# Kernel tuning notes

Hardware: AMD Instinct MI355X
Metric: run time of the kernel (lower is better)

Reference implementation:

```python
import jax, jax.numpy as jnp
import numpy as np

C = 384; NH = 12; HD = C // NH; MLP = int(C * 4.0)
B = 8; T = 12; N = 256; BT = B * T
EPS = 1e-6


def _ln(x):
    # LayerNorm without affine, eps=1e-6
    mu = jnp.mean(x, axis=-1, keepdims=True)
    var = jnp.mean(jnp.square(x - mu), axis=-1, keepdims=True)
    return (x - mu) / jnp.sqrt(var + EPS)


def _attention(x, wqkv, bqkv, wproj, bproj, bias=None):
    b, n, c = x.shape
    qkv = (x @ wqkv.T + bqkv).reshape(b, n, 3, NH, HD)
    q = qkv[:, :, 0].transpose(0, 2, 1, 3)  # [b,h,n,d]
    k = qkv[:, :, 1].transpose(0, 2, 1, 3)
    v = qkv[:, :, 2].transpose(0, 2, 1, 3)
    attn = jnp.einsum('bhnd,bhmd->bhnm', q, k) * (HD ** -0.5)
    if bias is not None:
        attn = attn + bias
    attn = jax.nn.softmax(attn, axis=-1)
    out = jnp.einsum('bhnm,bhmd->bhnd', attn, v).transpose(0, 2, 1, 3).reshape(b, n, c)
    return out @ wproj.T + bproj, attn


def setup_inputs() -> dict:
    key = jax.random.key(0)
    ks = jax.random.split(key, 20)
    s = 0.02
    inp = {
        'x': jax.random.normal(ks[0], (BT, N, C), jnp.float32),
        'c': jax.random.normal(ks[1], (BT, C), jnp.float32),
        'rel_pos_bias': jax.random.normal(ks[2], (1, NH, N, N), jnp.float32) * s,
        'w_adaln': jax.random.normal(ks[3], (9 * C, C), jnp.float32) * s,
        'b_adaln': jnp.zeros((9 * C,), jnp.float32),
        'wqkv_s': jax.random.normal(ks[4], (3 * C, C), jnp.float32) * s,
        'bqkv_s': jnp.zeros((3 * C,), jnp.float32),
        'wproj_s': jax.random.normal(ks[5], (C, C), jnp.float32) * s,
        'bproj_s': jnp.zeros((C,), jnp.float32),
        'wqkv_t': jax.random.normal(ks[6], (3 * C, C), jnp.float32) * s,
        'bqkv_t': jnp.zeros((3 * C,), jnp.float32),
        'wproj_t': jax.random.normal(ks[7], (C, C), jnp.float32) * s,
        'bproj_t': jnp.zeros((C,), jnp.float32),
        'w1': jax.random.normal(ks[8], (MLP, C), jnp.float32) * s,
        'b1': jnp.zeros((MLP,), jnp.float32),
        'w2': jax.random.normal(ks[9], (C, MLP), jnp.float32) * s,
        'b2': jnp.zeros((C,), jnp.float32),
        'T_pred': T,
    }
    return inp


def reference(x, c, rel_pos_bias, w_adaln, b_adaln, wqkv_s, bqkv_s, wproj_s, bproj_s,
              wqkv_t, bqkv_t, wproj_t, bproj_t, w1, b1, w2, b2, T_pred):
    mod = jax.nn.silu(c) @ w_adaln.T + b_adaln  # [BT, 9C]
    (shift_s, scale_s, gate_s, shift_t, scale_t, gate_t,
     shift_mlp, scale_mlp, gate_mlp) = jnp.split(mod, 9, axis=1)

    # spatial attention with adaLN modulate + gate
    x_mod = _ln(x) * (1 + scale_s[:, None]) + shift_s[:, None]
    x_s, attn_map = _attention(x_mod, wqkv_s, bqkv_s, wproj_s, bproj_s, bias=rel_pos_bias)
    x = x + gate_s[:, None] * x_s

    if T_pred > 1:
        bt, n, cdim = x.shape
        b = bt // T_pred
        xt = x.reshape(b, T_pred, n, cdim).transpose(0, 2, 1, 3).reshape(b * n, T_pred, cdim)
        sc = scale_t.reshape(b, 1, T_pred, cdim)
        sh = shift_t.reshape(b, 1, T_pred, cdim)
        gt = gate_t.reshape(b, 1, T_pred, cdim)
        norm_t = _ln(xt).reshape(b, n, T_pred, cdim)
        mod_t = (norm_t * (1 + sc) + sh).reshape(b * n, T_pred, cdim)
        x_t, _ = _attention(mod_t, wqkv_t, bqkv_t, wproj_t, bproj_t)
        x_t = (x_t.reshape(b, n, T_pred, cdim) * gt).transpose(0, 2, 1, 3).reshape(bt, n, cdim)
        x = x + x_t

    # gated MLP with exact (erf) GELU, matching nn.GELU default
    h = _ln(x) * (1 + scale_mlp[:, None]) + shift_mlp[:, None]
    h = jax.nn.gelu(h @ w1.T + b1, approximate=False) @ w2.T + b2
    x = x + gate_mlp[:, None] * h
    return (x, attn_map)
```

## Files before the change

### kernel.cpp

```cpp
#include <hip/hip_runtime.h>
#include <hip/hip_bf16.h>
#include <math.h>

typedef __bf16 bf16;
typedef __bf16 bf16x8 __attribute__((ext_vector_type(8)));
typedef __bf16 bf16x4 __attribute__((ext_vector_type(4)));
typedef float  f32x4  __attribute__((ext_vector_type(4)));

#define C_    384
#define NH_   12
#define HD_   32
#define MLP_  1536
#define B_    8
#define T_    12
#define N_    256
#define BT_   96
#define M_    24576
#define NINE_C 3456
#define QKV_  1152

#define GLOAD16(gptr, lptr)                                                \
  __builtin_amdgcn_global_load_lds(                                       \
      (const __attribute__((address_space(1))) void*)(gptr),              \
      (__attribute__((address_space(3))) void*)(lptr), 16, 0, 0)

__device__ __forceinline__ float wave_sum(float v) {
#pragma unroll
  for (int o = 32; o > 0; o >>= 1) v += __shfl_xor(v, o, 64);
  return v;
}

template <typename TO> __device__ __forceinline__ TO to_out(float v);
template <> __device__ __forceinline__ float to_out<float>(float v) { return v; }
template <> __device__ __forceinline__ bf16  to_out<bf16>(float v)  { return (bf16)v; }

struct F2BArgs {
  const float* src[7];
  bf16* dst[7];
  int n4[7];
};
__global__ __launch_bounds__(256) void k_f2b_all(F2BArgs a) {
  const int seg = blockIdx.y;
  const int i = blockIdx.x * 256 + threadIdx.x;
  if (i < a.n4[seg]) {
    float4 v = ((const float4*)a.src[seg])[i];
    bf16x4 o;
    o[0] = (bf16)v.x; o[1] = (bf16)v.y; o[2] = (bf16)v.z; o[3] = (bf16)v.w;
    ((bf16x4*)a.dst[seg])[i] = o;
  }
}

__global__ __launch_bounds__(384) void k_silu(const float* __restrict__ c,
                                              bf16* __restrict__ out) {
  const int row = blockIdx.x, tid = threadIdx.x;
  float v = 0.f;
  if (row < BT_) {
    float cv = c[row * C_ + tid];
    v = cv / (1.f + __expf(-cv));
  }
  out[row * C_ + tid] = (bf16)v;
}

__global__ __launch_bounds__(256) void k_ln_mod(const float* __restrict__ x,
                                                const float* __restrict__ mod,
                                                bf16* __restrict__ out,
                                                int shift_chunk, int scale_chunk) {
  const int wave = threadIdx.x >> 6, lane = threadIdx.x & 63;
  const int r = blockIdx.x * 4 + wave;
  const float* xr = x + (size_t)r * C_;
  float v[6];
  float s = 0.f, ss = 0.f;
#pragma unroll
  for (int e = 0; e < 6; ++e) { v[e] = xr[lane + 64 * e]; s += v[e]; ss += v[e] * v[e]; }
  s = wave_sum(s); ss = wave_sum(ss);
  const float mean = s * (1.f / C_);
  const float var  = ss * (1.f / C_) - mean * mean;
  const float rs   = rsqrtf(var + 1e-6f);
  const int bt = r >> 8;
  const float* sh = mod + (size_t)bt * NINE_C + shift_chunk * C_;
  const float* sc = mod + (size_t)bt * NINE_C + scale_chunk * C_;
  bf16* orow = out + (size_t)r * C_;
#pragma unroll
  for (int e = 0; e < 6; ++e) {
    int cc = lane + 64 * e;
    orow[cc] = (bf16)((v[e] - mean) * rs * (1.f + sc[cc]) + sh[cc]);
  }
}

__global__ __launch_bounds__(256) void k_ln_mod_t(const float* __restrict__ x,
                                                  const float* __restrict__ mod,
                                                  bf16* __restrict__ out) {
  const int wave = threadIdx.x >> 6, lane = threadIdx.x & 63;
  const int rr = blockIdx.x * 4 + wave;
  const int bn = rr / T_, t = rr - bn * T_;
  const int b = bn >> 8, n = bn & 255;
  const int in_row = (b * T_ + t) * N_ + n;
  const int mrow   = b * T_ + t;
  const float* xr = x + (size_t)in_row * C_;
  float v[6];
  float s = 0.f, ss = 0.f;
#pragma unroll
  for (int e = 0; e < 6; ++e) { v[e] = xr[lane + 64 * e]; s += v[e]; ss += v[e] * v[e]; }
  s = wave_sum(s); ss = wave_sum(ss);
  const float mean = s * (1.f / C_);
  const float var  = ss * (1.f / C_) - mean * mean;
  const float rs   = rsqrtf(var + 1e-6f);
  const float* sh = mod + (size_t)mrow * NINE_C + 3 * C_;
  const float* sc = mod + (size_t)mrow * NINE_C + 4 * C_;
  bf16* orow = out + (size_t)rr * C_;
#pragma unroll
  for (int e = 0; e < 6; ++e) {
    int cc = lane + 64 * e;
    orow[cc] = (bf16)((v[e] - mean) * rs * (1.f + sc[cc]) + sh[cc]);
  }
}

template <typename TO, int EPI>
__global__ __launch_bounds__(256) void mfma_gemm(const bf16* __restrict__ A,
                                                 const bf16* __restrict__ W,
                                                 const float* __restrict__ bias,
                                                 TO* __restrict__ out,
                                                 int M, int N, int K,
                                                 const float* __restrict__ base,
                                                 const float* __restrict__ mod,
                                                 int gc, int ntx) {
  __shared__ bf16 As[128 * 64];
  __shared__ bf16 Bs[128 * 64];
  const int tid = threadIdx.x;
  const int w = tid >> 6, l = tid & 63;
  const int nwg = gridDim.x;
  const int q8 = nwg >> 3, r8 = nwg & 7;
  const int xcd = blockIdx.x & 7, idx = blockIdx.x >> 3;
  const int t = (xcd < r8 ? xcd * (q8 + 1) : r8 * (q8 + 1) + (xcd - r8) * q8) + idx;
  const int m0 = (t / ntx) * 128, n0 = (t % ntx) * 128;
  const int wr = w >> 1, wc = w & 1;
  f32x4 acc[4][4];
#pragma unroll
  for (int mi = 0; mi < 4; ++mi)
#pragma unroll
    for (int nj = 0; nj < 4; ++nj) acc[mi][nj] = (f32x4){0.f, 0.f, 0.f, 0.f};

  const int srow8 = l >> 3;
  const int c8    = l & 7;

  for (int k0 = 0; k0 < K; k0 += 64) {
#pragma unroll
    for (int i = 0; i < 4; ++i) {
      int row = w * 32 + i * 8 + srow8;
      int sc = c8 ^ (row & 7);
      GLOAD16(A + (size_t)(m0 + row) * K + k0 + sc * 8,
              (char*)As + (w * 32 + i * 8) * 128);
      GLOAD16(W + (size_t)(n0 + row) * K + k0 + sc * 8,
              (char*)Bs + (w * 32 + i * 8) * 128);
    }
    __syncthreads();
#pragma unroll
    for (int kt = 0; kt < 2; ++kt) {
      bf16x8 a[4], b[4];
      const int cc = kt * 4 + (l >> 4);
#pragma unroll
      for (int mi = 0; mi < 4; ++mi) {
        int row = wr * 64 + mi * 16 + (l & 15);
        a[mi] = *(const bf16x8*)((const char*)As + row * 128 + ((cc ^ (row & 7)) << 4));
      }
#pragma unroll
      for (int nj = 0; nj < 4; ++nj) {
        int row = wc * 64 + nj * 16 + (l & 15);
        b[nj] = *(const bf16x8*)((const char*)Bs + row * 128 + ((cc ^ (row & 7)) << 4));
      }
#pragma unroll
      for (int mi = 0; mi < 4; ++mi)
#pragma unroll
        for (int nj = 0; nj < 4; ++nj)
          acc[mi][nj] = __builtin_amdgcn_mfma_f32_16x16x32_bf16(a[mi], b[nj], acc[mi][nj], 0, 0, 0);
    }
    __syncthreads();
  }
  const int btc = m0 >> 8;
#pragma unroll
  for (int nj = 0; nj < 4; ++nj) {
    int col = n0 + wc * 64 + nj * 16 + (l & 15);
    float bv = bias[col];
    float gv = 0.f;
    if (EPI == 2) gv = mod[(size_t)btc * NINE_C + gc * C_ + col];
#pragma unroll
    for (int mi = 0; mi < 4; ++mi) {
#pragma unroll
      for (int q = 0; q < 4; ++q) {
        int rrow = m0 + wr * 64 + mi * 16 + (l >> 4) * 4 + q;
        float v = acc[mi][nj][q] + bv;
        if (EPI == 0) {
          out[(size_t)rrow * N + col] = to_out<TO>(v);
        } else if (EPI == 1) {
          v = 0.5f * v * (1.f + erff(v * 0.70710678118654752f));
          out[(size_t)rrow * N + col] = to_out<TO>(v);
        } else if (EPI == 2) {
          ((float*)out)[(size_t)rrow * N + col] =
              base[(size_t)rrow * N + col] + gv * v;
        } else {
          int b = rrow / 3072;
          int rem = rrow - b * 3072;
          int n = rem / 12, tt = rem - n * 12;
          int btd = b * 12 + tt;
          size_t dst = ((size_t)btd * 256 + n) * N + col;
          float g = mod[(size_t)btd * NINE_C + 5 * C_ + col];
          ((float*)out)[dst] += g * v;
        }
      }
    }
  }
}

__global__ __launch_bounds__(256) void k_attn_fused(const bf16* __restrict__ qkv,
                                                    const float* __restrict__ bias,
                                                    float* __restrict__ attn,
                                                    bf16* __restrict__ out) {
  __shared__ bf16 Vt[32 * 256];
  __shared__ bf16 Pl[4][16][260];
  const int blk = blockIdx.x;
  const int bt = blk / NH_, h = blk - bt * NH_;
  const int tid = threadIdx.x;
#pragma unroll
  for (int r = 0; r < 4; ++r) {
    int id = tid + 256 * r;
    int j = id >> 2, c = id & 3;
    bf16x8 vv = *(const bf16x8*)(qkv + (size_t)(bt * N_ + j) * QKV_ + 2 * C_ + h * HD_ + c * 8);
    int kc = j >> 3, ke = j & 7;
#pragma unroll
    for (int i = 0; i < 8; ++i) {
      int d = c * 8 + i;
      *(bf16*)((char*)Vt + d * 512 + ((kc ^ (d & 7)) << 4) + ke * 2) = vv[i];
    }
  }
  const int w = tid >> 6, l = tid & 63;
  const int ln = l & 15, kg = l >> 4;
  const bf16* kbase = qkv + (size_t)bt * N_ * QKV_ + C_ + h * HD_ + kg * 8;
  bf16x8 kfr[16];
#pragma unroll
  for (int nj = 0; nj < 16; ++nj)
    kfr[nj] = *(const bf16x8*)(kbase + (size_t)(nj * 16 + ln) * QKV_);
  __syncthreads();

  const float scale = 0.17677669529663687f;
  const float* bb = bias + (size_t)h * N_ * N_;
  float* Pb = attn + (size_t)blk * N_ * N_;
  const bf16* qbase = qkv + (size_t)bt * N_ * QKV_ + h * HD_ + kg * 8;
  char* Pw = (char*)&Pl[w][0][0];

  for (int g = 0; g < 4; ++g) {
    const int i0 = w * 64 + g * 16;
    const int row = i0 + ln;
    bf16x8 aq = *(const bf16x8*)(qbase + (size_t)row * QKV_);
    f32x4 s[16];
#pragma unroll
    for (int nj = 0; nj < 16; ++nj)
      s[nj] = __builtin_amdgcn_mfma_f32_16x16x32_bf16(kfr[nj], aq, (f32x4){0.f,0.f,0.f,0.f}, 0, 0, 0);
    const float* brow = bb + (size_t)row * N_ + kg * 4;
    float v[16][4];
    float mx = -1e30f;
#pragma unroll
    for (int nj = 0; nj < 16; ++nj) {
      float4 bv = *(const float4*)(brow + nj * 16);
      v[nj][0] = s[nj][0] * scale + bv.x;
      v[nj][1] = s[nj][1] * scale + bv.y;
      v[nj][2] = s[nj][2] * scale + bv.z;
      v[nj][3] = s[nj][3] * scale + bv.w;
      mx = fmaxf(mx, fmaxf(fmaxf(v[nj][0], v[nj][1]), fmaxf(v[nj][2], v[nj][3])));
    }
    mx = fmaxf(mx, __shfl_xor(mx, 16, 64));
    mx = fmaxf(mx, __shfl_xor(mx, 32, 64));
    float sum = 0.f;
#pragma unroll
    for (int nj = 0; nj < 16; ++nj) {
      v[nj][0] = __expf(v[nj][0] - mx);
      v[nj][1] = __expf(v[nj][1] - mx);
      v[nj][2] = __expf(v[nj][2] - mx);
      v[nj][3] = __expf(v[nj][3] - mx);
      sum += (v[nj][0] + v[nj][1]) + (v[nj][2] + v[nj][3]);
    }
    sum += __shfl_xor(sum, 16, 64);
    sum += __shfl_xor(sum, 32, 64);
    const float inv = __frcp_rn(sum);
    float* prow = Pb + (size_t)row * N_ + kg * 4;
#pragma unroll
    for (int nj = 0; nj < 16; ++nj) {
      float4 o;
      o.x = v[nj][0] * inv; o.y = v[nj][1] * inv;
      o.z = v[nj][2] * inv; o.w = v[nj][3] * inv;
      *(float4*)(prow + nj * 16) = o;
      bf16x4 pb;
      pb[0] = (bf16)o.x; pb[1] = (bf16)o.y; pb[2] = (bf16)o.z; pb[3] = (bf16)o.w;
      *(bf16x4*)(Pw + ln * 520 + (nj * 16 + kg * 4) * 2) = pb;
    }
    f32x4 o0 = (f32x4){0.f,0.f,0.f,0.f}, o1 = (f32x4){0.f,0.f,0.f,0.f};
#pragma unroll
    for (int kt = 0; kt < 8; ++kt) {
      bf16x8 a = *(const bf16x8*)(Pw + ln * 520 + kt * 64 + kg * 16);
      int kc = kt * 4 + kg;
      bf16x8 b0 = *(const bf16x8*)((const char*)Vt + (size_t)ln * 512 + ((kc ^ (ln & 7)) << 4));
      bf16x8 b1 = *(const bf16x8*)((const char*)Vt + (size_t)(16 + ln) * 512 + ((kc ^ (ln & 7)) << 4));
      o0 = __builtin_amdgcn_mfma_f32_16x16x32_bf16(a, b0, o0, 0, 0, 0);
      o1 = __builtin_amdgcn_mfma_f32_16x16x32_bf16(a, b1, o1, 0, 0, 0);
    }
#pragma unroll
    for (int q = 0; q < 4; ++q) {
      int orow_i = i0 + kg * 4 + q;
      bf16* orow = out + (size_t)(bt * N_ + orow_i) * C_ + h * HD_;
      orow[ln]      = (bf16)o0[q];
      orow[16 + ln] = (bf16)o1[q];
    }
  }
}

__global__ __launch_bounds__(64) void k_attn_t(const bf16* __restrict__ qkv,
                                               bf16* __restrict__ out) {
  __shared__ float q[T_][HD_], k[T_][HD_], v[T_][HD_];
  const int blk = blockIdx.x;
  const int bn = blk / NH_, h = blk - bn * NH_;
  const int tid = threadIdx.x;
  for (int idx = tid; idx < T_ * 3 * HD_; idx += 64) {
    int t = idx / 96, rem = idx - t * 96;
    int s = rem >> 5, d = rem & 31;
    float val = (float)qkv[(size_t)(bn * T_ + t) * QKV_ + s * C_ + h * HD_ + d];
    if (s == 0) q[t][d] = val;
    else if (s == 1) k[t][d] = val;
    else v[t][d] = val;
  }
  __syncthreads();
  if (tid < T_) {
    const int i = tid;
    float sv[T_];
    float m = -1e30f;
#pragma unroll
    for (int j = 0; j < T_; ++j) {
      float s = 0.f;
#pragma unroll
      for (int d = 0; d < HD_; ++d) s += q[i][d] * k[j][d];
      s *= 0.17677669529663687f;
      sv[j] = s; m = fmaxf(m, s);
    }
    float l = 0.f;
#pragma unroll
    for (int j = 0; j < T_; ++j) { sv[j] = __expf(sv[j] - m); l += sv[j]; }
    const float inv = 1.f / l;
    float o[HD_];
#pragma unroll
    for (int d = 0; d < HD_; ++d) o[d] = 0.f;
#pragma unroll
    for (int j = 0; j < T_; ++j)
#pragma unroll
      for (int d = 0; d < HD_; ++d) o[d] += sv[j] * v[j][d];
    bf16* orow = out + (size_t)(bn * T_ + i) * C_ + h * HD_;
#pragma unroll
    for (int d = 0; d < HD_; ++d) orow[d] = (bf16)(o[d] * inv);
  }
}

extern "C" void kernel_launch(void* const* d_in, const int* in_sizes, int n_in,
                              void* d_out, int out_size, void* d_ws, size_t ws_size,
                              hipStream_t stream) {
  const float* x_in   = (const float*)d_in[0];
  const float* c_in   = (const float*)d_in[1];
  const float* relb   = (const float*)d_in[2];
  const float* w_ada  = (const float*)d_in[3];
  const float* b_ada  = (const float*)d_in[4];
  const float* wqkv_s = (const float*)d_in[5];
  const float* bqkv_s = (const float*)d_in[6];
  const float* wproj_s= (const float*)d_in[7];
  const float* bproj_s= (const float*)d_in[8];
  const float* wqkv_t = (const float*)d_in[9];
  const float* bqkv_t = (const float*)d_in[10];
  const float* wproj_t= (const float*)d_in[11];
  const float* bproj_t= (const float*)d_in[12];
  const float* w1     = (const float*)d_in[13];
  const float* b1     = (const float*)d_in[14];
  const float* w2     = (const float*)d_in[15];
  const float* b2     = (const float*)d_in[16];

  float* Xout = (float*)d_out;
  float* attn = (float*)d_out + (size_t)M_ * C_;

  char* ws = (char*)d_ws;
  float* mod    = (float*)ws;
  bf16*  silu_b = (bf16*)(ws + 1769472);
  bf16*  Wb     = (bf16*)(ws + 1867776);
  bf16*  Bbuf   = (bf16*)(ws + 9240576);
  bf16*  Abuf   = (bf16*)(ws + 28114944);

  bf16* wqkv_s_b  = Wb;
  bf16* wproj_s_b = Wb + 442368;
  bf16* wqkv_t_b  = Wb + 589824;
  bf16* wproj_t_b = Wb + 1032192;
  bf16* w1_b      = Wb + 1179648;
  bf16* w2_b      = Wb + 1769472;
  bf16* wada_b    = Wb + 2359296;

  F2BArgs fa;
  fa.src[0] = wqkv_s;  fa.dst[0] = wqkv_s_b;  fa.n4[0] = 110592;
  fa.src[1] = wproj_s; fa.dst[1] = wproj_s_b; fa.n4[1] = 36864;
  fa.src[2] = wqkv_t;  fa.dst[2] = wqkv_t_b;  fa.n4[2] = 110592;
  fa.src[3] = wproj_t; fa.dst[3] = wproj_t_b; fa.n4[3] = 36864;
  fa.src[4] = w1;      fa.dst[4] = w1_b;      fa.n4[4] = 147456;
  fa.src[5] = w2;      fa.dst[5] = w2_b;      fa.n4[5] = 147456;
  fa.src[6] = w_ada;   fa.dst[6] = wada_b;    fa.n4[6] = 331776;
  k_f2b_all<<<dim3(1296, 7), 256, 0, stream>>>(fa);

  k_silu<<<128, 384, 0, stream>>>(c_in, silu_b);
  mfma_gemm<float, 0><<<27, 256, 0, stream>>>(
      silu_b, wada_b, b_ada, mod, 128, NINE_C, C_, nullptr, nullptr, 0, 27);

  k_ln_mod<<<M_ / 4, 256, 0, stream>>>(x_in, mod, Bbuf, 0, 1);
  mfma_gemm<bf16, 0><<<(QKV_/128)*(M_/128), 256, 0, stream>>>(
      Bbuf, wqkv_s_b, bqkv_s, Abuf, M_, QKV_, C_, nullptr, nullptr, 0, QKV_/128);
  k_attn_fused<<<BT_ * NH_, 256, 0, stream>>>(Abuf, relb, attn, Bbuf);
  mfma_gemm<float, 2><<<(C_/128)*(M_/128), 256, 0, stream>>>(
      Bbuf, wproj_s_b, bproj_s, (float*)Xout, M_, C_, C_, x_in, mod, 2, C_/128);

  k_ln_mod_t<<<M_ / 4, 256, 0, stream>>>(Xout, mod, Bbuf);
  mfma_gemm<bf16, 0><<<(QKV_/128)*(M_/128), 256, 0, stream>>>(
      Bbuf, wqkv_t_b, bqkv_t, Abuf, M_, QKV_, C_, nullptr, nullptr, 0, QKV_/128);
  k_attn_t<<<B_ * N_ * NH_, 64, 0, stream>>>(Abuf, Bbuf);
  mfma_gemm<float, 3><<<(C_/128)*(M_/128), 256, 0, stream>>>(
      Bbuf, wproj_t_b, bproj_t, (float*)Xout, M_, C_, C_, nullptr, mod, 5, C_/128);

  k_ln_mod<<<M_ / 4, 256, 0, stream>>>(Xout, mod, Bbuf, 6, 7);
  mfma_gemm<bf16, 1><<<(MLP_/128)*(M_/128), 256, 0, stream>>>(
      Bbuf, w1_b, b1, Abuf, M_, MLP_, C_, nullptr, nullptr, 0, MLP_/128);
  mfma_gemm<float, 2><<<(C_/128)*(M_/128), 256, 0, stream>>>(
      Abuf, w2_b, b2, (float*)Xout, M_, C_, MLP_, Xout, mod, 8, C_/128);
}
```

Before: 504.9 us.

## Keep temporal path in natural row layout and fold silu into weight conversion

The temporal LN now reads rows in their original (bt,n) order through the shared k_ln_mod kernel. Temporal attention gathers q/k/v across the strided rows directly and writes back in natural order, so the projection GEMM can use a plain gated-residual epilogue instead of a scattered read-modify-write. The silu launch is merged into the weight bf16-conversion kernel, LN loads and stores are vectorised to float2, and the attention-map and final output writes use nontemporal stores. The cost is strided, less coalesced qkv gathers and output writes in the small temporal attention kernel.

```diff
diff --git a/kernel.cpp b/kernel.cpp
--- a/kernel.cpp
+++ b/kernel.cpp
@@ -35,30 +35,32 @@
 template <> __device__ __forceinline__ bf16  to_out<bf16>(float v)  { return (bf16)v; }
 
 struct F2BArgs {
-  const float* src[7];
-  bf16* dst[7];
-  int n4[7];
+  const float* src[8];
+  bf16* dst[8];
+  int n4[8];
 };
 __global__ __launch_bounds__(256) void k_f2b_all(F2BArgs a) {
   const int seg = blockIdx.y;
   const int i = blockIdx.x * 256 + threadIdx.x;
-  if (i < a.n4[seg]) {
-    float4 v = ((const float4*)a.src[seg])[i];
+  if (i >= a.n4[seg]) return;
+  if (seg == 7) {
     bf16x4 o;
-    o[0] = (bf16)v.x; o[1] = (bf16)v.y; o[2] = (bf16)v.z; o[3] = (bf16)v.w;
-    ((bf16x4*)a.dst[seg])[i] = o;
-  }
-}
-
-__global__ __launch_bounds__(384) void k_silu(const float* __restrict__ c,
-                                              bf16* __restrict__ out) {
-  const int row = blockIdx.x, tid = threadIdx.x;
-  float v = 0.f;
-  if (row < BT_) {
-    float cv = c[row * C_ + tid];
-    v = cv / (1.f + __expf(-cv));
-  }
-  out[row * C_ + tid] = (bf16)v;
+    if (i < 9216) {
+      float4 v = ((const float4*)a.src[7])[i];
+      o[0] = (bf16)(v.x / (1.f + __expf(-v.x)));
+      o[1] = (bf16)(v.y / (1.f + __expf(-v.y)));
+      o[2] = (bf16)(v.z / (1.f + __expf(-v.z)));
+      o[3] = (bf16)(v.w / (1.f + __expf(-v.w)));
+    } else {
+      o[0] = o[1] = o[2] = o[3] = (bf16)0.f;
+    }
+    ((bf16x4*)a.dst[7])[i] = o;
+    return;
+  }
+  float4 v = ((const float4*)a.src[seg])[i];
+  bf16x4 o;
+  o[0] = (bf16)v.x; o[1] = (bf16)v.y; o[2] = (bf16)v.z; o[3] = (bf16)v.w;
+  ((bf16x4*)a.dst[seg])[i] = o;
 }
 
 __global__ __launch_bounds__(256) void k_ln_mod(const float* __restrict__ x,
@@ -68,10 +70,14 @@
   const int wave = threadIdx.x >> 6, lane = threadIdx.x & 63;
   const int r = blockIdx.x * 4 + wave;
   const float* xr = x + (size_t)r * C_;
-  float v[6];
+  float2 v[3];
   float s = 0.f, ss = 0.f;
 #pragma unroll
-  for (int e = 0; e < 6; ++e) { v[e] = xr[lane + 64 * e]; s += v[e]; ss += v[e] * v[e]; }
+  for (int e = 0; e < 3; ++e) {
+    v[e] = *(const float2*)&xr[lane * 2 + 128 * e];
+    s += v[e].x + v[e].y;
+    ss += v[e].x * v[e].x + v[e].y * v[e].y;
+  }
   s = wave_sum(s); ss = wave_sum(ss);
   const float mean = s * (1.f / C_);
   const float var  = ss * (1.f / C_) - mean * mean;
@@ -81,37 +87,14 @@
   const float* sc = mod + (size_t)bt * NINE_C + scale_chunk * C_;
   bf16* orow = out + (size_t)r * C_;
 #pragma unroll
-  for (int e = 0; e < 6; ++e) {
-    int cc = lane + 64 * e;
-    orow[cc] = (bf16)((v[e] - mean) * rs * (1.f + sc[cc]) + sh[cc]);
-  }
-}
-
-__global__ __launch_bounds__(256) void k_ln_mod_t(const float* __restrict__ x,
-                                                  const float* __restrict__ mod,
-                                                  bf16* __restrict__ out) {
-  const int wave = threadIdx.x >> 6, lane = threadIdx.x & 63;
-  const int rr = blockIdx.x * 4 + wave;
-  const int bn = rr / T_, t = rr - bn * T_;
-  const int b = bn >> 8, n = bn & 255;
-  const int in_row = (b * T_ + t) * N_ + n;
-  const int mrow   = b * T_ + t;
-  const float* xr = x + (size_t)in_row * C_;
-  float v[6];
-  float s = 0.f, ss = 0.f;
-#pragma unroll
-  for (int e = 0; e < 6; ++e) { v[e] = xr[lane + 64 * e]; s += v[e]; ss += v[e] * v[e]; }
-  s = wave_sum(s); ss = wave_sum(ss);
-  const float mean = s * (1.f / C_);
-  const float var  = ss * (1.f / C_) - mean * mean;
-  const float rs   = rsqrtf(var + 1e-6f);
-  const float* sh = mod + (size_t)mrow * NINE_C + 3 * C_;
-  const float* sc = mod + (size_t)mrow * NINE_C + 4 * C_;
-  bf16* orow = out + (size_t)rr * C_;
-#pragma unroll
-  for (int e = 0; e < 6; ++e) {
-    int cc = lane + 64 * e;
-    orow[cc] = (bf16)((v[e] - mean) * rs * (1.f + sc[cc]) + sh[cc]);
+  for (int e = 0; e < 3; ++e) {
+    int cc = lane * 2 + 128 * e;
+    float2 s2 = *(const float2*)&sc[cc];
+    float2 h2 = *(const float2*)&sh[cc];
+    union { bf16 b[2]; unsigned u; } pk;
+    pk.b[0] = (bf16)((v[e].x - mean) * rs * (1.f + s2.x) + h2.x);
+    pk.b[1] = (bf16)((v[e].y - mean) * rs * (1.f + s2.y) + h2.y);
+    *(unsigned*)&orow[cc] = pk.u;
   }
 }
 
@@ -182,7 +165,7 @@
     int col = n0 + wc * 64 + nj * 16 + (l & 15);
     float bv = bias[col];
     float gv = 0.f;
-    if (EPI == 2) gv = mod[(size_t)btc * NINE_C + gc * C_ + col];
+    if (EPI == 2 || EPI == 4) gv = mod[(size_t)btc * NINE_C + gc * C_ + col];
 #pragma unroll
     for (int mi = 0; mi < 4; ++mi) {
 #pragma unroll
@@ -198,13 +181,8 @@
           ((float*)out)[(size_t)rrow * N + col] =
               base[(size_t)rrow * N + col] + gv * v;
         } else {
-          int b = rrow / 3072;
-          int rem = rrow - b * 3072;
-          int n = rem / 12, tt = rem - n * 12;
-          int btd = b * 12 + tt;
-          size_t dst = ((size_t)btd * 256 + n) * N + col;
-          float g = mod[(size_t)btd * NINE_C + 5 * C_ + col];
-          ((float*)out)[dst] += g * v;
+          float o = base[(size_t)rrow * N + col] + gv * v;
+          __builtin_nontemporal_store(o, &((float*)out)[(size_t)rrow * N + col]);
         }
       }
     }
@@ -284,12 +262,12 @@
     float* prow = Pb + (size_t)row * N_ + kg * 4;
 #pragma unroll
     for (int nj = 0; nj < 16; ++nj) {
-      float4 o;
-      o.x = v[nj][0] * inv; o.y = v[nj][1] * inv;
-      o.z = v[nj][2] * inv; o.w = v[nj][3] * inv;
-      *(float4*)(prow + nj * 16) = o;
+      f32x4 o;
+      o[0] = v[nj][0] * inv; o[1] = v[nj][1] * inv;
+      o[2] = v[nj][2] * inv; o[3] = v[nj][3] * inv;
+      __builtin_nontemporal_store(o, (f32x4*)(prow + nj * 16));
       bf16x4 pb;
-      pb[0] = (bf16)o.x; pb[1] = (bf16)o.y; pb[2] = (bf16)o.z; pb[3] = (bf16)o.w;
+      pb[0] = (bf16)o[0]; pb[1] = (bf16)o[1]; pb[2] = (bf16)o[2]; pb[3] = (bf16)o[3];
       *(bf16x4*)(Pw + ln * 520 + (nj * 16 + kg * 4) * 2) = pb;
     }
     f32x4 o0 = (f32x4){0.f,0.f,0.f,0.f}, o1 = (f32x4){0.f,0.f,0.f,0.f};
@@ -317,11 +295,13 @@
   __shared__ float q[T_][HD_], k[T_][HD_], v[T_][HD_];
   const int blk = blockIdx.x;
   const int bn = blk / NH_, h = blk - bn * NH_;
+  const int b = bn >> 8, n = bn & 255;
   const int tid = threadIdx.x;
   for (int idx = tid; idx < T_ * 3 * HD_; idx += 64) {
     int t = idx / 96, rem = idx - t * 96;
     int s = rem >> 5, d = rem & 31;
-    float val = (float)qkv[(size_t)(bn * T_ + t) * QKV_ + s * C_ + h * HD_ + d];
+    const int row = (b * T_ + t) * N_ + n;
+    float val = (float)qkv[(size_t)row * QKV_ + s * C_ + h * HD_ + d];
     if (s == 0) q[t][d] = val;
     else if (s == 1) k[t][d] = val;
     else v[t][d] = val;
@@ -350,7 +330,7 @@
     for (int j = 0; j < T_; ++j)
 #pragma unroll
       for (int d = 0; d < HD_; ++d) o[d] += sv[j] * v[j][d];
-    bf16* orow = out + (size_t)(bn * T_ + i) * C_ + h * HD_;
+    bf16* orow = out + (size_t)((b * T_ + i) * N_ + n) * C_ + h * HD_;
 #pragma unroll
     for (int d = 0; d < HD_; ++d) orow[d] = (bf16)(o[d] * inv);
   }
@@ -403,9 +383,9 @@
   fa.src[4] = w1;      fa.dst[4] = w1_b;      fa.n4[4] = 147456;
   fa.src[5] = w2;      fa.dst[5] = w2_b;      fa.n4[5] = 147456;
   fa.src[6] = w_ada;   fa.dst[6] = wada_b;    fa.n4[6] = 331776;
-  k_f2b_all<<<dim3(1296, 7), 256, 0, stream>>>(fa);
-
-  k_silu<<<128, 384, 0, stream>>>(c_in, silu_b);
+  fa.src[7] = c_in;    fa.dst[7] = silu_b;    fa.n4[7] = 12288;
+  k_f2b_all<<<dim3(1296, 8), 256, 0, stream>>>(fa);
+
   mfma_gemm<float, 0><<<27, 256, 0, stream>>>(
       silu_b, wada_b, b_ada, mod, 128, NINE_C, C_, nullptr, nullptr, 0, 27);
 
@@ -416,16 +396,16 @@
   mfma_gemm<float, 2><<<(C_/128)*(M_/128), 256, 0, stream>>>(
       Bbuf, wproj_s_b, bproj_s, (float*)Xout, M_, C_, C_, x_in, mod, 2, C_/128);
 
-  k_ln_mod_t<<<M_ / 4, 256, 0, stream>>>(Xout, mod, Bbuf);
+  k_ln_mod<<<M_ / 4, 256, 0, stream>>>(Xout, mod, Bbuf, 3, 4);
   mfma_gemm<bf16, 0><<<(QKV_/128)*(M_/128), 256, 0, stream>>>(
       Bbuf, wqkv_t_b, bqkv_t, Abuf, M_, QKV_, C_, nullptr, nullptr, 0, QKV_/128);
   k_attn_t<<<B_ * N_ * NH_, 64, 0, stream>>>(Abuf, Bbuf);
-  mfma_gemm<float, 3><<<(C_/128)*(M_/128), 256, 0, stream>>>(
-      Bbuf, wproj_t_b, bproj_t, (float*)Xout, M_, C_, C_, nullptr, mod, 5, C_/128);
+  mfma_gemm<float, 2><<<(C_/128)*(M_/128), 256, 0, stream>>>(
+      Bbuf, wproj_t_b, bproj_t, (float*)Xout, M_, C_, C_, Xout, mod, 5, C_/128);
 
   k_ln_mod<<<M_ / 4, 256, 0, stream>>>(Xout, mod, Bbuf, 6, 7);
   mfma_gemm<bf16, 1><<<(MLP_/128)*(M_/128), 256, 0, stream>>>(
       Bbuf, w1_b, b1, Abuf, M_, MLP_, C_, nullptr, nullptr, 0, MLP_/128);
-  mfma_gemm<float, 2><<<(C_/128)*(M_/128), 256, 0, stream>>>(
+  mfma_gemm<float, 4><<<(C_/128)*(M_/128), 256, 0, stream>>>(
       Abuf, w2_b, b2, (float*)Xout, M_, C_, MLP_, Xout, mod, 8, C_/128);
 }
```

Result: faster. 446.2 us (-11.6%).
